# Optimization experiments

Hardware: AMD Instinct MI355X
Metric: run time of the kernel (lower is better)

## Reference

```python
import jax, jax.numpy as jnp
import numpy as np


def setup_inputs() -> dict:
    key = jax.random.key(0)
    k1, k2, k3 = jax.random.split(key, 3)
    S, G, B, C, P = 3, 8, 2048, 512, 64
    node_feats = jax.random.normal(k1, (S, G * B, C), dtype=jnp.float32)
    weight = jax.random.normal(k2, (P, C), dtype=jnp.float32)
    smooth_factor = jax.random.normal(k3, (P,), dtype=jnp.float32)
    return {
        "node_feats": node_feats,
        "weight": weight,
        "smooth_factor": smooth_factor,
        "batch_size": B,
        "num_graphs": G,
    }


def reference(node_feats, weight, smooth_factor, batch_size, num_graphs):
    # node_feats: [S, N_scale, C] (scales stacked; torch version takes a list and cats)
    S, Ns, C = node_feats.shape
    P = weight.shape[0]
    x = node_feats.reshape(-1, C)                       # [N, C], N = S*Ns

    # RBF-style score: (2*c.x - |x|^2 - |c|^2), clamped at 0, scaled by beta
    cx = x @ weight.T                                   # [N, P]
    x_sq = jnp.sum(x * x, axis=1, keepdims=True)        # [N, 1]
    c_sq = jnp.sum(weight * weight, axis=1)[None, :]    # [1, P]
    beta = jax.nn.sigmoid(smooth_factor)                # [P]
    logits = jnp.minimum(2.0 * cx - x_sq - c_sq, 0.0) / beta[None, :]
    assign = jax.nn.softmax(logits, axis=1)             # [N, P]

    # Per-graph weighted sum (uniform batch_list), accumulated across scales:
    # out[g] = sum_{s,n in graph g} assign[s,g,n]^T feats[s,g,n]
    a = assign.reshape(S, num_graphs, batch_size, P)
    f = node_feats.reshape(S, num_graphs, batch_size, C)
    outputs = jnp.einsum('sgnp,sgnc->gpc', a, f)        # [G, P, C]
    return outputs, assign
```

## Files before the change

kernel.cpp:

```cpp
#include <hip/hip_runtime.h>
#include <math.h>

#define S_ 3
#define G_ 8
#define B_ 2048
#define C_ 512
#define P_ 64
#define N_ (S_ * G_ * B_)

typedef __attribute__((ext_vector_type(8))) short short8;
typedef __attribute__((ext_vector_type(4))) float f32x4;
typedef __attribute__((ext_vector_type(4))) unsigned int uint4v;
typedef __attribute__((ext_vector_type(2))) unsigned int uint2v;

__device__ __forceinline__ unsigned f2bf1(float f) {
    union { float f; unsigned u; } c; c.f = f;
    unsigned u = c.u;
    u += 0x7fffu + ((u >> 16) & 1u);
    return u >> 16;
}
__device__ __forceinline__ unsigned pk2(float a, float b) {
    return f2bf1(a) | (f2bf1(b) << 16);
}

__global__ void zero_kernel(float* __restrict__ out) {
    int i = blockIdx.x * blockDim.x + threadIdx.x;
    ((f32x4*)out)[i] = (f32x4){0.f, 0.f, 0.f, 0.f};
}

__global__ __launch_bounds__(64) void prep_kernel(
    const float* __restrict__ w, const float* __restrict__ sf,
    unsigned short* __restrict__ wb, float* __restrict__ csq,
    float* __restrict__ rbeta)
{
    const int p = blockIdx.x, l = threadIdx.x;
    const float* wr = w + (size_t)p * C_ + l * 8;
    f32x4 a = *(const f32x4*)wr;
    f32x4 b = *(const f32x4*)(wr + 4);
    float s = a[0]*a[0] + a[1]*a[1] + a[2]*a[2] + a[3]*a[3]
            + b[0]*b[0] + b[1]*b[1] + b[2]*b[2] + b[3]*b[3];
    uint4v pk;
    pk.x = pk2(a[0], a[1]); pk.y = pk2(a[2], a[3]);
    pk.z = pk2(b[0], b[1]); pk.w = pk2(b[2], b[3]);
    *(uint4v*)&wb[(size_t)p * C_ + l * 8] = pk;
#pragma unroll
    for (int off = 1; off < 64; off <<= 1) s += __shfl_xor(s, off, 64);
    if (l == 0) csq[p] = s;
    if (p == 0) rbeta[l] = 1.0f + expf(-sf[l]);
}

#define XSTR 72
#define NSTR 66

__global__ __launch_bounds__(256, 3) void assign_v5(
    const float* __restrict__ x, const unsigned short* __restrict__ wb,
    const float* __restrict__ csq, const float* __restrict__ rbeta,
    float* __restrict__ assign, unsigned short* __restrict__ a_t)
{
    __shared__ __align__(16) char smem[64 * XSTR * 2 * 2];
    unsigned short* xs  = (unsigned short*)smem;
    unsigned short* wsh = (unsigned short*)(smem + 64 * XSTR * 2);
    float* lg = (float*)smem;
    __shared__ float xsq_s[64];

    const int t = threadIdx.x, lane = t & 63, wv = t >> 6;
    const int q = lane >> 4, col = lane & 15;
    const int n0 = blockIdx.x * 64;
    const int srow = t >> 4, sseg = t & 15;
    const int wp = t >> 3, wseg = t & 7;

    float csqv[4], rbv[4];
#pragma unroll
    for (int nt = 0; nt < 4; ++nt) {
        csqv[nt] = csq[16 * nt + col];
        rbv[nt]  = rbeta[16 * nt + col];
    }

    f32x4 acc[4];
#pragma unroll
    for (int nt = 0; nt < 4; ++nt) acc[nt] = (f32x4){0.f, 0.f, 0.f, 0.f};
    float xacc[4] = {0.f, 0.f, 0.f, 0.f};

    f32x4 xr[2][4]; uint4v wr[2][2];
#pragma unroll
    for (int i = 0; i < 4; ++i)
        xr[0][i] = *(const f32x4*)(x + (size_t)(n0 + srow + 16 * i) * C_ + sseg * 4);
#pragma unroll
    for (int i = 0; i < 2; ++i)
        wr[0][i] = *(const uint4v*)&wb[(size_t)(wp + 32 * i) * C_ + wseg * 8];

#pragma unroll
    for (int ch = 0; ch < 8; ++ch) {
        const int cur = ch & 1, nxt = cur ^ 1;
        if (ch) __syncthreads();
#pragma unroll
        for (int i = 0; i < 4; ++i) {
            f32x4 v = xr[cur][i];
            xacc[i] += v.x*v.x + v.y*v.y + v.z*v.z + v.w*v.w;
            uint2v u; u.x = pk2(v.x, v.y); u.y = pk2(v.z, v.w);
            *(uint2v*)&xs[(srow + 16 * i) * XSTR + sseg * 4] = u;
        }
#pragma unroll
        for (int i = 0; i < 2; ++i)
            *(uint4v*)&wsh[(wp + 32 * i) * XSTR + wseg * 8] = wr[cur][i];
        if (ch < 7) {
            const int k0 = (ch + 1) * 64;
#pragma unroll
            for (int i = 0; i < 4; ++i)
                xr[nxt][i] = *(const f32x4*)(x + (size_t)(n0 + srow + 16 * i) * C_ + k0 + sseg * 4);
#pragma unroll
            for (int i = 0; i < 2; ++i)
                wr[nxt][i] = *(const uint4v*)&wb[(size_t)(wp + 32 * i) * C_ + k0 + wseg * 8];
        }
        __syncthreads();
#pragma unroll
        for (int s = 0; s < 2; ++s) {
            const int koff = s * 32 + q * 8;
            short8 af = *(const short8*)&xs[(16 * wv + col) * XSTR + koff];
#pragma unroll
            for (int nt = 0; nt < 4; ++nt) {
                short8 bf = *(const short8*)&wsh[(16 * nt + col) * XSTR + koff];
                acc[nt] = __builtin_amdgcn_mfma_f32_16x16x32_bf16(af, bf, acc[nt], 0, 0, 0);
            }
        }
    }

#pragma unroll
    for (int i = 0; i < 4; ++i) {
#pragma unroll
        for (int off = 1; off < 16; off <<= 1)
            xacc[i] += __shfl_xor(xacc[i], off, 64);
    }
    if ((lane & 15) == 0) {
#pragma unroll
        for (int i = 0; i < 4; ++i) xsq_s[srow + 16 * i] = xacc[i];
    }
    __syncthreads();

    float vals[4][4];
#pragma unroll
    for (int reg = 0; reg < 4; ++reg) {
        const int row = 16 * wv + 4 * q + reg;
        const float xq = xsq_s[row];
        float vmax = -3.4e38f;
#pragma unroll
        for (int nt = 0; nt < 4; ++nt) {
            float v = 2.0f * acc[nt][reg] - xq - csqv[nt];
            v = fminf(v, 0.0f) * rbv[nt];
            vals[reg][nt] = v;
            vmax = fmaxf(vmax, v);
        }
#pragma unroll
        for (int off = 1; off < 16; off <<= 1)
            vmax = fmaxf(vmax, __shfl_xor(vmax, off, 64));
        float ss = 0.f;
#pragma unroll
        for (int nt = 0; nt < 4; ++nt) { vals[reg][nt] = __expf(vals[reg][nt] - vmax); ss += vals[reg][nt]; }
#pragma unroll
        for (int off = 1; off < 16; off <<= 1)
            ss += __shfl_xor(ss, off, 64);
        const float inv = 1.0f / ss;
#pragma unroll
        for (int nt = 0; nt < 4; ++nt) vals[reg][nt] *= inv;
    }
    __syncthreads();

#pragma unroll
    for (int reg = 0; reg < 4; ++reg) {
        const int row = 16 * wv + 4 * q + reg;
#pragma unroll
        for (int nt = 0; nt < 4; ++nt) {
            lg[row * 68 + 16 * nt + col] = vals[reg][nt];
            assign[(size_t)(n0 + row) * P_ + 16 * nt + col] = vals[reg][nt];
        }
    }
    __syncthreads();

    const int p = lane;
    float v[16];
#pragma unroll
    for (int i = 0; i < 16; ++i) v[i] = lg[(wv * 16 + i) * 68 + p];
    uint4v d0, d1;
    d0.x = pk2(v[0], v[1]);   d0.y = pk2(v[2], v[3]);
    d0.z = pk2(v[4], v[5]);   d0.w = pk2(v[6], v[7]);
    d1.x = pk2(v[8], v[9]);   d1.y = pk2(v[10], v[11]);
    d1.z = pk2(v[12], v[13]); d1.w = pk2(v[14], v[15]);
    unsigned short* dst = a_t + (size_t)p * N_ + n0 + wv * 16;
    *(uint4v*)dst = d0;
    *(uint4v*)(dst + 8) = d1;
}

__global__ __launch_bounds__(256, 3) void group_v5(
    const float* __restrict__ x, const unsigned short* __restrict__ a_t,
    float* __restrict__ out)
{
    __shared__ __align__(16) unsigned short ash[64 * XSTR];
    __shared__ __align__(16) unsigned short xsn[64 * NSTR];

    const int t = threadIdx.x, lane = t & 63, wv = t >> 6;
    const int q = lane >> 4, col = lane & 15;
    const int g = blockIdx.x, c0 = blockIdx.y * 64, ks = blockIdx.z;
    const int sc = ks >> 2, b0 = (ks & 3) * 512;
    const size_t base = (size_t)sc * (G_ * B_) + (size_t)g * B_ + b0;
    const int ap = t >> 3, aseg = t & 7;
    const int srow = t >> 4, sseg = t & 15;

    f32x4 acc[4];
#pragma unroll
    for (int mt = 0; mt < 4; ++mt) acc[mt] = (f32x4){0.f, 0.f, 0.f, 0.f};

    uint4v ar[2][2]; f32x4 xr[2][4];
#pragma unroll
    for (int i = 0; i < 2; ++i)
        ar[0][i] = *(const uint4v*)&a_t[(size_t)(ap + 32 * i) * N_ + base + aseg * 8];
#pragma unroll
    for (int i = 0; i < 4; ++i)
        xr[0][i] = *(const f32x4*)(x + (base + srow + 16 * i) * C_ + c0 + sseg * 4);

#pragma unroll
    for (int ch = 0; ch < 8; ++ch) {
        const int cur = ch & 1, nxt = cur ^ 1;
        if (ch) __syncthreads();
#pragma unroll
        for (int i = 0; i < 2; ++i)
            *(uint4v*)&ash[(ap + 32 * i) * XSTR + aseg * 8] = ar[cur][i];
#pragma unroll
        for (int i = 0; i < 4; ++i) {
            f32x4 v = xr[cur][i];
            uint2v u; u.x = pk2(v.x, v.y); u.y = pk2(v.z, v.w);
            *(uint2v*)&xsn[(srow + 16 * i) * NSTR + sseg * 4] = u;
        }
        if (ch < 7) {
            const int nb = (ch + 1) * 64;
#pragma unroll
            for (int i = 0; i < 2; ++i)
                ar[nxt][i] = *(const uint4v*)&a_t[(size_t)(ap + 32 * i) * N_ + base + nb + aseg * 8];
#pragma unroll
            for (int i = 0; i < 4; ++i)
                xr[nxt][i] = *(const f32x4*)(x + (base + nb + srow + 16 * i) * C_ + c0 + sseg * 4);
        }
        __syncthreads();
#pragma unroll
        for (int s = 0; s < 2; ++s) {
            const int koff = s * 32 + q * 8;
            short8 bfr;
#pragma unroll
            for (int j = 0; j < 8; ++j)
                bfr[j] = xsn[(koff + j) * NSTR + 16 * wv + col];
#pragma unroll
            for (int mt = 0; mt < 4; ++mt) {
                short8 afr = *(const short8*)&ash[(16 * mt + col) * XSTR + koff];
                acc[mt] = __builtin_amdgcn_mfma_f32_16x16x32_bf16(afr, bfr, acc[mt], 0, 0, 0);
            }
        }
    }

#pragma unroll
    for (int mt = 0; mt < 4; ++mt) {
#pragma unroll
        for (int reg = 0; reg < 4; ++reg) {
            const int p = 16 * mt + 4 * q + reg;
            const int c = c0 + 16 * wv + col;
            atomicAdd(&out[(size_t)g * (P_ * C_) + (size_t)p * C_ + c], acc[mt][reg]);
        }
    }
}

extern "C" void kernel_launch(void* const* d_in, const int* in_sizes, int n_in,
                              void* d_out, int out_size, void* d_ws, size_t ws_size,
                              hipStream_t stream) {
    const float* x  = (const float*)d_in[0];
    const float* w  = (const float*)d_in[1];
    const float* sf = (const float*)d_in[2];

    float* out    = (float*)d_out;
    float* assign = out + (size_t)G_ * P_ * C_;

    unsigned short* wb    = (unsigned short*)d_ws;
    float*          csq   = (float*)((char*)d_ws + 65536);
    float*          rbeta = (float*)((char*)d_ws + 65792);
    unsigned short* a_t   = (unsigned short*)((char*)d_ws + 66048);

    zero_kernel<<<(G_ * P_ * C_) / (4 * 256), 256, 0, stream>>>(out);
    prep_kernel<<<P_, 64, 0, stream>>>(w, sf, wb, csq, rbeta);
    assign_v5<<<N_ / 64, 256, 0, stream>>>(x, wb, csq, rbeta, assign, a_t);
    dim3 gridB(G_, C_ / 64, 12);
    group_v5<<<gridB, 256, 0, stream>>>(x, a_t, out);
}
```

Before: 188.7 us.

## Stream fp32 tiles via global_load_lds with swizzle; replace atomics with partial reduction

Both the assign and group kernels now load fp32 x tiles straight from global memory into LDS with global_load_lds, using an XOR swizzle to limit bank conflicts. The bf16 conversion and the squared-norm accumulation move to the LDS read side, which removes register staging and the per-chunk second barrier. The group kernel writes per-split partial tiles to workspace instead of atomically adding into a zeroed output, and a new reduce kernel sums the 12 splits. This drops the zero kernel and the atomics, at the cost of double-buffered fp32 LDS (more LDS per block, which may lower occupancy) and an extra kernel launch with more workspace traffic.

```diff
diff --git a/kernel.cpp b/kernel.cpp
--- a/kernel.cpp
+++ b/kernel.cpp
@@ -11,7 +11,6 @@
 typedef __attribute__((ext_vector_type(8))) short short8;
 typedef __attribute__((ext_vector_type(4))) float f32x4;
 typedef __attribute__((ext_vector_type(4))) unsigned int uint4v;
-typedef __attribute__((ext_vector_type(2))) unsigned int uint2v;
 
 __device__ __forceinline__ unsigned f2bf1(float f) {
     union { float f; unsigned u; } c; c.f = f;
@@ -22,10 +21,10 @@
 __device__ __forceinline__ unsigned pk2(float a, float b) {
     return f2bf1(a) | (f2bf1(b) << 16);
 }
-
-__global__ void zero_kernel(float* __restrict__ out) {
-    int i = blockIdx.x * blockDim.x + threadIdx.x;
-    ((f32x4*)out)[i] = (f32x4){0.f, 0.f, 0.f, 0.f};
+__device__ __forceinline__ void gl_lds16(const void* g, void* l) {
+    __builtin_amdgcn_global_load_lds(
+        (const __attribute__((address_space(1))) void*)g,
+        (__attribute__((address_space(3))) void*)l, 16, 0, 0);
 }
 
 __global__ __launch_bounds__(64) void prep_kernel(
@@ -49,25 +48,30 @@
     if (p == 0) rbeta[l] = 1.0f + expf(-sf[l]);
 }
 
-#define XSTR 72
-#define NSTR 66
-
-__global__ __launch_bounds__(256, 3) void assign_v5(
+__global__ __launch_bounds__(256, 3) void assign_v6(
     const float* __restrict__ x, const unsigned short* __restrict__ wb,
     const float* __restrict__ csq, const float* __restrict__ rbeta,
     float* __restrict__ assign, unsigned short* __restrict__ a_t)
 {
-    __shared__ __align__(16) char smem[64 * XSTR * 2 * 2];
-    unsigned short* xs  = (unsigned short*)smem;
-    unsigned short* wsh = (unsigned short*)(smem + 64 * XSTR * 2);
-    float* lg = (float*)smem;
+    __shared__ __align__(16) float xsb[2][64 * 64];
+    __shared__ __align__(16) unsigned short wsb[2][64 * 72];
     __shared__ float xsq_s[64];
+    float* lg = &xsb[0][0];
 
     const int t = threadIdx.x, lane = t & 63, wv = t >> 6;
     const int q = lane >> 4, col = lane & 15;
     const int n0 = blockIdx.x * 64;
-    const int srow = t >> 4, sseg = t & 15;
+    const int ro = lane >> 4, sslot = lane & 15;
     const int wp = t >> 3, wseg = t & 7;
+
+    const float* gx[4];
+#pragma unroll
+    for (int i = 0; i < 4; ++i) {
+        const int row = 16 * wv + 4 * i + ro;
+        const int pr  = ((row >> 1) & 7) | (row & 8);
+        gx[i] = x + (size_t)(n0 + row) * C_ + ((sslot ^ pr) << 2);
+    }
+    const int prA = ((col >> 1) & 7) | (col & 8);
 
     float csqv[4], rbv[4];
 #pragma unroll
@@ -79,62 +83,49 @@
     f32x4 acc[4];
 #pragma unroll
     for (int nt = 0; nt < 4; ++nt) acc[nt] = (f32x4){0.f, 0.f, 0.f, 0.f};
-    float xacc[4] = {0.f, 0.f, 0.f, 0.f};
-
-    f32x4 xr[2][4]; uint4v wr[2][2];
-#pragma unroll
-    for (int i = 0; i < 4; ++i)
-        xr[0][i] = *(const f32x4*)(x + (size_t)(n0 + srow + 16 * i) * C_ + sseg * 4);
-#pragma unroll
-    for (int i = 0; i < 2; ++i)
-        wr[0][i] = *(const uint4v*)&wb[(size_t)(wp + 32 * i) * C_ + wseg * 8];
+    float xsq = 0.f;
+
+    uint4v wr0 = *(const uint4v*)&wb[(size_t)wp * C_ + wseg * 8];
+    uint4v wr1 = *(const uint4v*)&wb[(size_t)(wp + 32) * C_ + wseg * 8];
+#pragma unroll
+    for (int i = 0; i < 4; ++i) gl_lds16(gx[i], &xsb[0][(16 * wv + 4 * i) * 64]);
 
 #pragma unroll
     for (int ch = 0; ch < 8; ++ch) {
-        const int cur = ch & 1, nxt = cur ^ 1;
-        if (ch) __syncthreads();
-#pragma unroll
-        for (int i = 0; i < 4; ++i) {
-            f32x4 v = xr[cur][i];
-            xacc[i] += v.x*v.x + v.y*v.y + v.z*v.z + v.w*v.w;
-            uint2v u; u.x = pk2(v.x, v.y); u.y = pk2(v.z, v.w);
-            *(uint2v*)&xs[(srow + 16 * i) * XSTR + sseg * 4] = u;
-        }
-#pragma unroll
-        for (int i = 0; i < 2; ++i)
-            *(uint4v*)&wsh[(wp + 32 * i) * XSTR + wseg * 8] = wr[cur][i];
+        const int cur = ch & 1;
+        *(uint4v*)&wsb[cur][wp * 72 + wseg * 8]        = wr0;
+        *(uint4v*)&wsb[cur][(wp + 32) * 72 + wseg * 8] = wr1;
+        __syncthreads();
         if (ch < 7) {
             const int k0 = (ch + 1) * 64;
+            wr0 = *(const uint4v*)&wb[(size_t)wp * C_ + k0 + wseg * 8];
+            wr1 = *(const uint4v*)&wb[(size_t)(wp + 32) * C_ + k0 + wseg * 8];
 #pragma unroll
             for (int i = 0; i < 4; ++i)
-                xr[nxt][i] = *(const f32x4*)(x + (size_t)(n0 + srow + 16 * i) * C_ + k0 + sseg * 4);
-#pragma unroll
-            for (int i = 0; i < 2; ++i)
-                wr[nxt][i] = *(const uint4v*)&wb[(size_t)(wp + 32 * i) * C_ + k0 + wseg * 8];
-        }
-        __syncthreads();
+                gl_lds16(gx[i] + k0, &xsb[cur ^ 1][(16 * wv + 4 * i) * 64]);
+        }
 #pragma unroll
         for (int s = 0; s < 2; ++s) {
+            const int g0 = 8 * s + 2 * q;
+            f32x4 f0 = *(const f32x4*)&xsb[cur][(16 * wv + col) * 64 + ((g0 ^ prA) << 2)];
+            f32x4 f1 = *(const f32x4*)&xsb[cur][(16 * wv + col) * 64 + (((g0 + 1) ^ prA) << 2)];
+            xsq += f0.x*f0.x + f0.y*f0.y + f0.z*f0.z + f0.w*f0.w
+                 + f1.x*f1.x + f1.y*f1.y + f1.z*f1.z + f1.w*f1.w;
+            union { uint4v u; short8 s8; } cv;
+            cv.u.x = pk2(f0.x, f0.y); cv.u.y = pk2(f0.z, f0.w);
+            cv.u.z = pk2(f1.x, f1.y); cv.u.w = pk2(f1.z, f1.w);
             const int koff = s * 32 + q * 8;
-            short8 af = *(const short8*)&xs[(16 * wv + col) * XSTR + koff];
 #pragma unroll
             for (int nt = 0; nt < 4; ++nt) {
-                short8 bf = *(const short8*)&wsh[(16 * nt + col) * XSTR + koff];
-                acc[nt] = __builtin_amdgcn_mfma_f32_16x16x32_bf16(af, bf, acc[nt], 0, 0, 0);
+                short8 bf = *(const short8*)&wsb[cur][(16 * nt + col) * 72 + koff];
+                acc[nt] = __builtin_amdgcn_mfma_f32_16x16x32_bf16(cv.s8, bf, acc[nt], 0, 0, 0);
             }
         }
     }
 
-#pragma unroll
-    for (int i = 0; i < 4; ++i) {
-#pragma unroll
-        for (int off = 1; off < 16; off <<= 1)
-            xacc[i] += __shfl_xor(xacc[i], off, 64);
-    }
-    if ((lane & 15) == 0) {
-#pragma unroll
-        for (int i = 0; i < 4; ++i) xsq_s[srow + 16 * i] = xacc[i];
-    }
+    xsq += __shfl_xor(xsq, 16, 64);
+    xsq += __shfl_xor(xsq, 32, 64);
+    if (q == 0) xsq_s[16 * wv + col] = xsq;
     __syncthreads();
 
     float vals[4][4];
@@ -163,7 +154,6 @@
 #pragma unroll
         for (int nt = 0; nt < 4; ++nt) vals[reg][nt] *= inv;
     }
-    __syncthreads();
 
 #pragma unroll
     for (int reg = 0; reg < 4; ++reg) {
@@ -190,80 +180,99 @@
     *(uint4v*)(dst + 8) = d1;
 }
 
-__global__ __launch_bounds__(256, 3) void group_v5(
+__global__ __launch_bounds__(256, 3) void group_v6(
     const float* __restrict__ x, const unsigned short* __restrict__ a_t,
-    float* __restrict__ out)
-{
-    __shared__ __align__(16) unsigned short ash[64 * XSTR];
-    __shared__ __align__(16) unsigned short xsn[64 * NSTR];
+    float* __restrict__ part)
+{
+    __shared__ __align__(16) float xsb[2][64 * 64];
+    __shared__ __align__(16) unsigned short asb[2][64 * 64];
 
     const int t = threadIdx.x, lane = t & 63, wv = t >> 6;
     const int q = lane >> 4, col = lane & 15;
-    const int g = blockIdx.x, c0 = blockIdx.y * 64, ks = blockIdx.z;
-    const int sc = ks >> 2, b0 = (ks & 3) * 512;
+    const int g = blockIdx.x, ct = blockIdx.y, ks = blockIdx.z;
+    const int c0 = ct * 64, sc = ks >> 2, b0 = (ks & 3) * 512;
     const size_t base = (size_t)sc * (G_ * B_) + (size_t)g * B_ + b0;
-    const int ap = t >> 3, aseg = t & 7;
-    const int srow = t >> 4, sseg = t & 15;
+    const int ro = lane >> 4, sslot = lane & 15;
+    const int aro = lane >> 3, aseg = lane & 7;
+
+    const float* gx[4];
+#pragma unroll
+    for (int i = 0; i < 4; ++i) {
+        const int n  = 16 * wv + 4 * i + ro;
+        const int pm = ((n >> 3) & 3) | (((n >> 3) & 1) << 2);
+        gx[i] = x + (base + n) * C_ + c0 + ((sslot ^ pm) << 2);
+    }
+    const unsigned short* ga[2];
+#pragma unroll
+    for (int i = 0; i < 2; ++i) {
+        const int p = 16 * wv + 8 * i + aro;
+        ga[i] = a_t + (size_t)p * N_ + base + aseg * 8;
+    }
+    const int cl = 16 * wv + col;
+    const int permq = q | ((q & 1) << 2);
+    const int cswz  = (((cl >> 2) ^ permq) << 2) | (cl & 3);
 
     f32x4 acc[4];
 #pragma unroll
     for (int mt = 0; mt < 4; ++mt) acc[mt] = (f32x4){0.f, 0.f, 0.f, 0.f};
 
-    uint4v ar[2][2]; f32x4 xr[2][4];
-#pragma unroll
-    for (int i = 0; i < 2; ++i)
-        ar[0][i] = *(const uint4v*)&a_t[(size_t)(ap + 32 * i) * N_ + base + aseg * 8];
-#pragma unroll
-    for (int i = 0; i < 4; ++i)
-        xr[0][i] = *(const f32x4*)(x + (base + srow + 16 * i) * C_ + c0 + sseg * 4);
+#pragma unroll
+    for (int i = 0; i < 4; ++i) gl_lds16(gx[i], &xsb[0][(16 * wv + 4 * i) * 64]);
+#pragma unroll
+    for (int i = 0; i < 2; ++i) gl_lds16(ga[i], &asb[0][(16 * wv + 8 * i) * 64]);
 
 #pragma unroll
     for (int ch = 0; ch < 8; ++ch) {
-        const int cur = ch & 1, nxt = cur ^ 1;
-        if (ch) __syncthreads();
-#pragma unroll
-        for (int i = 0; i < 2; ++i)
-            *(uint4v*)&ash[(ap + 32 * i) * XSTR + aseg * 8] = ar[cur][i];
-#pragma unroll
-        for (int i = 0; i < 4; ++i) {
-            f32x4 v = xr[cur][i];
-            uint2v u; u.x = pk2(v.x, v.y); u.y = pk2(v.z, v.w);
-            *(uint2v*)&xsn[(srow + 16 * i) * NSTR + sseg * 4] = u;
-        }
+        const int cur = ch & 1;
+        __syncthreads();
         if (ch < 7) {
             const int nb = (ch + 1) * 64;
 #pragma unroll
+            for (int i = 0; i < 4; ++i)
+                gl_lds16(gx[i] + (size_t)nb * C_, &xsb[cur ^ 1][(16 * wv + 4 * i) * 64]);
+#pragma unroll
             for (int i = 0; i < 2; ++i)
-                ar[nxt][i] = *(const uint4v*)&a_t[(size_t)(ap + 32 * i) * N_ + base + nb + aseg * 8];
-#pragma unroll
-            for (int i = 0; i < 4; ++i)
-                xr[nxt][i] = *(const f32x4*)(x + (base + nb + srow + 16 * i) * C_ + c0 + sseg * 4);
-        }
-        __syncthreads();
+                gl_lds16(ga[i] + nb, &asb[cur ^ 1][(16 * wv + 8 * i) * 64]);
+        }
 #pragma unroll
         for (int s = 0; s < 2; ++s) {
             const int koff = s * 32 + q * 8;
-            short8 bfr;
-#pragma unroll
-            for (int j = 0; j < 8; ++j)
-                bfr[j] = xsn[(koff + j) * NSTR + 16 * wv + col];
+            float gv[8];
+#pragma unroll
+            for (int j = 0; j < 8; ++j) gv[j] = xsb[cur][(koff + j) * 64 + cswz];
+            union { uint4v u; short8 s8; } cv;
+            cv.u.x = pk2(gv[0], gv[1]); cv.u.y = pk2(gv[2], gv[3]);
+            cv.u.z = pk2(gv[4], gv[5]); cv.u.w = pk2(gv[6], gv[7]);
 #pragma unroll
             for (int mt = 0; mt < 4; ++mt) {
-                short8 afr = *(const short8*)&ash[(16 * mt + col) * XSTR + koff];
-                acc[mt] = __builtin_amdgcn_mfma_f32_16x16x32_bf16(afr, bfr, acc[mt], 0, 0, 0);
+                short8 af = *(const short8*)&asb[cur][(16 * mt + col) * 64 + koff];
+                acc[mt] = __builtin_amdgcn_mfma_f32_16x16x32_bf16(af, cv.s8, acc[mt], 0, 0, 0);
             }
         }
     }
 
-#pragma unroll
-    for (int mt = 0; mt < 4; ++mt) {
+    float* pt = part + (((size_t)(g * 8 + ct) * 12) + ks) * 4096;
+#pragma unroll
+    for (int mt = 0; mt < 4; ++mt)
 #pragma unroll
         for (int reg = 0; reg < 4; ++reg) {
             const int p = 16 * mt + 4 * q + reg;
-            const int c = c0 + 16 * wv + col;
-            atomicAdd(&out[(size_t)g * (P_ * C_) + (size_t)p * C_ + c], acc[mt][reg]);
-        }
-    }
+            pt[p * 64 + cl] = acc[mt][reg];
+        }
+}
+
+__global__ __launch_bounds__(256) void reduce_out(
+    const float* __restrict__ part, float* __restrict__ out)
+{
+    const int idx = blockIdx.x * 256 + threadIdx.x;
+    const int g = idx >> 15, r = idx & 32767;
+    const int p = r >> 9,  c = r & 511;
+    const int ct = c >> 6, cl = c & 63;
+    const float* src = part + (((size_t)(g * 8 + ct) * 12)) * 4096 + p * 64 + cl;
+    float s = 0.f;
+#pragma unroll
+    for (int ks = 0; ks < 12; ++ks) s += src[(size_t)ks * 4096];
+    out[idx] = s;
 }
 
 extern "C" void kernel_launch(void* const* d_in, const int* in_sizes, int n_in,
@@ -280,10 +289,11 @@
     float*          csq   = (float*)((char*)d_ws + 65536);
     float*          rbeta = (float*)((char*)d_ws + 65792);
     unsigned short* a_t   = (unsigned short*)((char*)d_ws + 66048);
-
-    zero_kernel<<<(G_ * P_ * C_) / (4 * 256), 256, 0, stream>>>(out);
+    float*          part  = (float*)((char*)d_ws + 6553600);
+
     prep_kernel<<<P_, 64, 0, stream>>>(w, sf, wb, csq, rbeta);
-    assign_v5<<<N_ / 64, 256, 0, stream>>>(x, wb, csq, rbeta, assign, a_t);
+    assign_v6<<<N_ / 64, 256, 0, stream>>>(x, wb, csq, rbeta, assign, a_t);
     dim3 gridB(G_, C_ / 64, 12);
-    group_v5<<<gridB, 256, 0, stream>>>(x, a_t, out);
-}
+    group_v6<<<gridB, 256, 0, stream>>>(x, a_t, part);
+    reduce_out<<<(G_ * P_ * C_) / 256, 256, 0, stream>>>(part, out);
+}
```

Result: no change. 185.3 us (-1.8%).
